# Kernel optimization log

Measured on AMD Instinct MI355X. Metric: run time of the kernel, lower is better.

The kernel has to match this reference:

```python
import math
import jax, jax.numpy as jnp
import numpy as np

B, S, D, H = 2, 2048, 2048, 16  # batch, seq, d_model, n_heads


def setup_inputs() -> dict:
    key = jax.random.key(0)
    ks = jax.random.split(key, 5)
    w_scale = 1.0 / math.sqrt(D)
    return {
        "x": jax.random.normal(ks[0], (B, S, D), jnp.float32),
        "attn_bias": jax.random.normal(ks[1], (1, H, S, S), jnp.float32) * 0.1,
        "Wqkv_w": jax.random.normal(ks[2], (3 * D, D), jnp.float32) * w_scale,
        "Wqkv_b": jnp.zeros((3 * D,), jnp.float32),
        "out_w": jax.random.normal(ks[3], (D, D), jnp.float32) * w_scale,
        "out_b": jnp.zeros((D,), jnp.float32),
    }


def reference(x, attn_bias, Wqkv_w, Wqkv_b, out_w, out_b):
    b, s, d = x.shape
    hd = d // H                      # head dim = 128
    scale = 1.0 / math.sqrt(hd)      # module default: 1/sqrt(d_model // n_heads)

    # fused QKV projection
    qkv = x @ Wqkv_w.T + Wqkv_b                       # [b, s, 3d]
    q, k, v = jnp.split(qkv, 3, axis=2)               # each [b, s, d]
    q = q.reshape(b, s, H, hd).transpose(0, 2, 1, 3)  # [b, h, s, hd]
    k = k.reshape(b, s, H, hd).transpose(0, 2, 1, 3)
    v = v.reshape(b, s, H, hd).transpose(0, 2, 1, 3)

    # scaled scores + additive bias (bias sliced to trailing q/k lengths)
    scores = jnp.einsum('bhqd,bhkd->bhqk', q, k) * scale
    scores = scores + attn_bias[:, :, -s:, -s:]

    # causal mask, masked positions set to dtype min (matches masked_fill with finfo.min)
    causal = jnp.tril(jnp.ones((s, s), dtype=bool))   # True = keep
    min_val = jnp.finfo(scores.dtype).min
    scores = jnp.where(causal[None, None, :, :], scores, min_val)

    p = jax.nn.softmax(scores, axis=-1)               # [b, h, s, s]
    out = jnp.einsum('bhqk,bhkd->bhqd', p, v)         # [b, h, s, hd]
    out = out.transpose(0, 2, 1, 3).reshape(b, s, d)  # [b, s, d]

    return out @ out_w.T + out_b
```

## Files before the change

### kernel.cpp

```cpp
#include <hip/hip_runtime.h>
#include <hip/hip_bf16.h>
#include <stdint.h>

#define H_  16
#define S_  2048
#define D_  2048
#define HD_ 128

typedef __bf16 bf16x8 __attribute__((ext_vector_type(8)));
typedef short  s16x8  __attribute__((ext_vector_type(8)));
typedef float  f32x4  __attribute__((ext_vector_type(4)));
typedef unsigned short u16x4 __attribute__((ext_vector_type(4)));

__device__ __forceinline__ unsigned short f2bf(float f) {
    unsigned u = __builtin_bit_cast(unsigned, f);
    u += 0x7fffu + ((u >> 16) & 1u);
    return (unsigned short)(u >> 16);
}

__device__ __forceinline__ bf16x8 ld_bf8(const unsigned short* p) {
    s16x8 r = *reinterpret_cast<const s16x8*>(p);
    return __builtin_bit_cast(bf16x8, r);
}

#define GLOAD_LDS16(gp, lp)                                                     \
    __builtin_amdgcn_global_load_lds(                                            \
        (const __attribute__((address_space(1))) void*)(gp),                     \
        (__attribute__((address_space(3))) void*)(lp), 16, 0, 0)

__global__ __launch_bounds__(256) void cast_f32_bf16(const float* __restrict__ in,
                                                     unsigned short* __restrict__ out,
                                                     int n) {
    int i = (blockIdx.x * 256 + threadIdx.x) * 4;
    if (i >= n) return;
    float4 v = *reinterpret_cast<const float4*>(in + i);
    u16x4 o;
    o[0] = f2bf(v.x); o[1] = f2bf(v.y); o[2] = f2bf(v.z); o[3] = f2bf(v.w);
    *reinterpret_cast<u16x4*>(out + i) = o;
}

__global__ __launch_bounds__(256) void gemm_bt_qkv(const unsigned short* __restrict__ A,
                                                   const unsigned short* __restrict__ W,
                                                   const float* __restrict__ bias,
                                                   unsigned short* __restrict__ Qo,
                                                   unsigned short* __restrict__ Ko,
                                                   unsigned short* __restrict__ Vo) {
    __shared__ alignas(16) unsigned short As[128 * 32];
    __shared__ alignas(16) unsigned short Bs[128 * 32];
    const int t  = threadIdx.x;
    const int l  = t & 63, w = t >> 6;
    const int wr = w >> 1, wc = w & 1;
    const int lr = l & 15, g = l >> 4;

    const int GX = 48, NWG = 1536, CPX = NWG / 8;
    const int raw = blockIdx.y * GX + blockIdx.x;
    const int swz = (raw & 7) * CPX + (raw >> 3);
    const int m0 = (swz / GX) * 128, n0 = (swz % GX) * 128;
    const int Kd = D_;

    f32x4 zero = {0.f, 0.f, 0.f, 0.f};
    f32x4 acc[4][4];
    for (int i = 0; i < 4; ++i)
        for (int j = 0; j < 4; ++j) acc[i][j] = zero;

    const int ea = t * 8;
    const int rowA = ea >> 5, colA = ea & 31;

    for (int kt = 0; kt < Kd; kt += 32) {
        GLOAD_LDS16(A + (size_t)(m0 + rowA) * Kd + kt + colA, &As[ea]);
        GLOAD_LDS16(A + (size_t)(m0 + 64 + rowA) * Kd + kt + colA, &As[2048 + ea]);
        GLOAD_LDS16(W + (size_t)(n0 + rowA) * Kd + kt + colA, &Bs[ea]);
        GLOAD_LDS16(W + (size_t)(n0 + 64 + rowA) * Kd + kt + colA, &Bs[2048 + ea]);
        __syncthreads();
        bf16x8 af[4], bfr[4];
        for (int mi = 0; mi < 4; ++mi) af[mi]  = ld_bf8(&As[(wr * 64 + mi * 16 + lr) * 32 + g * 8]);
        for (int ni = 0; ni < 4; ++ni) bfr[ni] = ld_bf8(&Bs[(wc * 64 + ni * 16 + lr) * 32 + g * 8]);
        for (int mi = 0; mi < 4; ++mi)
            for (int ni = 0; ni < 4; ++ni)
                acc[mi][ni] = __builtin_amdgcn_mfma_f32_16x16x32_bf16(af[mi], bfr[ni], acc[mi][ni], 0, 0, 0);
        __syncthreads();
    }

    for (int mi = 0; mi < 4; ++mi) {
        for (int ni = 0; ni < 4; ++ni) {
            for (int i = 0; i < 4; ++i) {
                int m = m0 + wr * 64 + mi * 16 + g * 4 + i;
                int n = n0 + wc * 64 + ni * 16 + lr;
                float v = acc[mi][ni][i] + bias[n];
                int which = n >> 11;
                int n2 = n & 2047;
                int h = n2 >> 7, d = n2 & 127;
                int b = m >> 11, s = m & 2047;
                unsigned short bv = f2bf(v);
                if (which == 0)
                    Qo[(((size_t)(b * H_ + h)) * S_ + s) * HD_ + d] = bv;
                else if (which == 1)
                    Ko[(((size_t)(b * H_ + h)) * S_ + s) * HD_ + d] = bv;
                else
                    Vo[(((size_t)(b * H_ + h)) * HD_ + d) * S_ + s] = bv;
            }
        }
    }
}

__global__ __launch_bounds__(256) void attn_kernel10(const unsigned short* __restrict__ Q,
                                                     const unsigned short* __restrict__ K,
                                                     const unsigned short* __restrict__ Vt,
                                                     const float* __restrict__ biasPtr,
                                                     unsigned short* __restrict__ O) {
    __shared__ alignas(16) unsigned short Klds[2][4096];
    __shared__ alignas(16) unsigned short Vlds[2][4096];
    __shared__ alignas(16) unsigned short Pbuf[4][16 * 32];

    const int t  = threadIdx.x;
    const int l  = t & 63, w = t >> 6;
    const int lr = l & 15, g = l >> 4;

    const int raw   = blockIdx.x;
    const int xcd   = raw & 7;
    const int local = raw >> 3;
    const int cu    = local & 31;
    const int slot  = local >> 5;
    const int qt    = (slot & 1) ? cu : (31 - cu);
    const int bh    = xcd + 8 * slot;
    const int b     = bh >> 4, head = bh & 15;

    const unsigned short* Qb = Q + (size_t)bh * S_ * HD_;
    const unsigned short* Kb = K + (size_t)bh * S_ * HD_;
    const unsigned short* Vb = Vt + (size_t)bh * HD_ * S_;
    const float* Bh32 = biasPtr + (size_t)head * S_ * S_;
    const float scale = 0.08838834764831845f;

    const int q0 = qt * 64 + w * 16;

    bf16x8 qf[4];
#pragma unroll
    for (int dc = 0; dc < 4; ++dc)
        qf[dc] = ld_bf8(Qb + (size_t)(q0 + lr) * HD_ + dc * 32 + g * 8);

    f32x4 zero = {0.f, 0.f, 0.f, 0.f};
    f32x4 o[8];
#pragma unroll
    for (int nc = 0; nc < 8; ++nc) o[nc] = zero;
    float lp[4] = {0.f, 0.f, 0.f, 0.f};

    unsigned short* Pw = Pbuf[w];

    auto STAGE = [&](int buf, int k0) {
#pragma unroll
        for (int p = 0; p < 2; ++p) {
            int lin = p * 4096 + t * 16;
            int row = lin >> 8;
            int colb = lin & 255;
            int scolb = colb ^ ((row & 7) << 4);
            GLOAD_LDS16(Kb + (size_t)(k0 + row) * HD_ + (scolb >> 1), &Klds[buf][lin >> 1]);
        }
#pragma unroll
        for (int p = 0; p < 2; ++p) {
            int lin = p * 4096 + t * 16;
            int row = lin >> 6;
            int colb = lin & 63;
            int scolb = colb ^ ((row & 3) << 4);
            GLOAD_LDS16(Vb + (size_t)row * S_ + k0 + (scolb >> 1), &Vlds[buf][lin >> 1]);
        }
    };

    STAGE(0, 0);
    __syncthreads();

    const int nch = 2 * qt + 2;
    int cur = 0;
    for (int c = 0; c < nch; ++c) {
        const int k0 = c * 32;

        if (c + 1 < nch) STAGE(cur ^ 1, k0 + 32);

        float bias_r[4][2];
#pragma unroll
        for (int i = 0; i < 4; ++i) {
            const int boff = (q0 + g * 4 + i) * S_ + k0 + lr;
#pragma unroll
            for (int kc = 0; kc < 2; ++kc)
                bias_r[i][kc] = Bh32[boff + kc * 16];
        }

        f32x4 s[2];
        s[0] = zero; s[1] = zero;
#pragma unroll
        for (int kc = 0; kc < 2; ++kc) {
            bf16x8 kf[4];
#pragma unroll
            for (int dc = 0; dc < 4; ++dc)
                kf[dc] = ld_bf8(&Klds[cur][(kc * 16 + lr) * 128 + ((dc * 32 + g * 8) ^ ((lr & 7) << 3))]);
#pragma unroll
            for (int dc = 0; dc < 4; ++dc)
                s[kc] = __builtin_amdgcn_mfma_f32_16x16x32_bf16(qf[dc], kf[dc], s[kc], 0, 0, 0);
        }

        const bool maskzone = (c >= nch - 2);
#pragma unroll
        for (int i = 0; i < 4; ++i) {
            const int rowabs = q0 + g * 4 + i;
            const int prow   = g * 4 + i;
            float e[2];
#pragma unroll
            for (int kc = 0; kc < 2; ++kc) {
                float v = s[kc][i] * scale + bias_r[i][kc];
                if (maskzone && (k0 + kc * 16 + lr > rowabs)) v = -1.0e30f;
                e[kc] = __expf(v - 16.0f);
            }
            lp[i] += e[0] + e[1];
            const int sw = (prow & 3) << 3;
            Pw[(prow * 32 + 0  + lr) ^ sw] = f2bf(e[0]);
            Pw[(prow * 32 + 16 + lr) ^ sw] = f2bf(e[1]);
        }

        {
            bf16x8 pa = ld_bf8(&Pw[lr * 32 + ((g * 8) ^ ((lr & 3) << 3))]);
#pragma unroll
            for (int nc = 0; nc < 8; ++nc) {
                bf16x8 vf = ld_bf8(&Vlds[cur][(nc * 16 + lr) * 32 + ((g * 8) ^ ((lr & 3) << 3))]);
                o[nc] = __builtin_amdgcn_mfma_f32_16x16x32_bf16(pa, vf, o[nc], 0, 0, 0);
            }
        }

        __syncthreads();
        cur ^= 1;
    }

#pragma unroll
    for (int i = 0; i < 4; ++i) {
        lp[i] += __shfl_xor(lp[i], 1);
        lp[i] += __shfl_xor(lp[i], 2);
        lp[i] += __shfl_xor(lp[i], 4);
        lp[i] += __shfl_xor(lp[i], 8);
    }

#pragma unroll
    for (int i = 0; i < 4; ++i) {
        float inv = 1.0f / lp[i];
        int row = q0 + g * 4 + i;
#pragma unroll
        for (int nc = 0; nc < 8; ++nc) {
            O[((size_t)(b * S_ + row)) * D_ + head * HD_ + nc * 16 + lr] = f2bf(o[nc][i] * inv);
        }
    }
}

__global__ __launch_bounds__(256) void gemm_bt_out(const unsigned short* __restrict__ A,
                                                   const unsigned short* __restrict__ W,
                                                   const float* __restrict__ bias,
                                                   float* __restrict__ out) {
    __shared__ alignas(16) unsigned short As[128 * 32];
    __shared__ alignas(16) unsigned short Bs[128 * 32];
    const int t  = threadIdx.x;
    const int l  = t & 63, w = t >> 6;
    const int wr = w >> 1, wc = w & 1;
    const int lr = l & 15, g = l >> 4;

    const int GX = 16, NWG = 512, CPX = NWG / 8;
    const int raw = blockIdx.y * GX + blockIdx.x;
    const int swz = (raw & 7) * CPX + (raw >> 3);
    const int m0 = (swz / GX) * 128, n0 = (swz % GX) * 128;
    const int Kd = D_;

    f32x4 zero = {0.f, 0.f, 0.f, 0.f};
    f32x4 acc[4][4];
    for (int i = 0; i < 4; ++i)
        for (int j = 0; j < 4; ++j) acc[i][j] = zero;

    const int ea = t * 8;
    const int rowA = ea >> 5, colA = ea & 31;

    for (int kt = 0; kt < Kd; kt += 32) {
        GLOAD_LDS16(A + (size_t)(m0 + rowA) * Kd + kt + colA, &As[ea]);
        GLOAD_LDS16(A + (size_t)(m0 + 64 + rowA) * Kd + kt + colA, &As[2048 + ea]);
        GLOAD_LDS16(W + (size_t)(n0 + rowA) * Kd + kt + colA, &Bs[ea]);
        GLOAD_LDS16(W + (size_t)(n0 + 64 + rowA) * Kd + kt + colA, &Bs[2048 + ea]);
        __syncthreads();
        bf16x8 af[4], bfr[4];
        for (int mi = 0; mi < 4; ++mi) af[mi]  = ld_bf8(&As[(wr * 64 + mi * 16 + lr) * 32 + g * 8]);
        for (int ni = 0; ni < 4; ++ni) bfr[ni] = ld_bf8(&Bs[(wc * 64 + ni * 16 + lr) * 32 + g * 8]);
        for (int mi = 0; mi < 4; ++mi)
            for (int ni = 0; ni < 4; ++ni)
                acc[mi][ni] = __builtin_amdgcn_mfma_f32_16x16x32_bf16(af[mi], bfr[ni], acc[mi][ni], 0, 0, 0);
        __syncthreads();
    }

    for (int mi = 0; mi < 4; ++mi) {
        for (int ni = 0; ni < 4; ++ni) {
            for (int i = 0; i < 4; ++i) {
                int m = m0 + wr * 64 + mi * 16 + g * 4 + i;
                int n = n0 + wc * 64 + ni * 16 + lr;
                out[(size_t)m * D_ + n] = acc[mi][ni][i] + bias[n];
            }
        }
    }
}

extern "C" void kernel_launch(void* const* d_in, const int* in_sizes, int n_in,
                              void* d_out, int out_size, void* d_ws, size_t ws_size,
                              hipStream_t stream) {
    (void)in_sizes; (void)n_in; (void)out_size; (void)ws_size;
    const float* x         = (const float*)d_in[0];
    const float* attn_bias = (const float*)d_in[1];
    const float* Wqkv_w    = (const float*)d_in[2];
    const float* Wqkv_b    = (const float*)d_in[3];
    const float* out_w     = (const float*)d_in[4];
    const float* out_b     = (const float*)d_in[5];
    float* out = (float*)d_out;

    char* ws = (char*)d_ws;
    unsigned short* xb    = (unsigned short*)(ws);
    unsigned short* wqkvb = (unsigned short*)(ws + 16777216);
    unsigned short* woutb = (unsigned short*)(ws + 41943040);
    unsigned short* Qb    = (unsigned short*)(ws + 50331648);
    unsigned short* Kb    = (unsigned short*)(ws + 67108864);
    unsigned short* Vtb   = (unsigned short*)(ws + 83886080);
    unsigned short* Ob    = xb;

    cast_f32_bf16<<<8192, 256, 0, stream>>>(x, xb, 8388608);
    cast_f32_bf16<<<12288, 256, 0, stream>>>(Wqkv_w, wqkvb, 12582912);
    cast_f32_bf16<<<4096, 256, 0, stream>>>(out_w, woutb, 4194304);
    gemm_bt_qkv<<<dim3(48, 32), 256, 0, stream>>>(xb, wqkvb, Wqkv_b, Qb, Kb, Vtb);
    attn_kernel10<<<1024, 256, 0, stream>>>(Qb, Kb, Vtb, attn_bias, Ob);
    gemm_bt_out<<<dim3(16, 32), 256, 0, stream>>>(Ob, woutb, out_b, out);
}
```

Before: 325.2 us.

## Rewrite GEMMs with triple-buffered async LDS pipeline, swizzled layout, larger tiles

Both projection GEMMs now share a core that loads 64-wide K slices into three rotating LDS buffers through global_load_lds. It waits with partial vmcnt, so global loads for two tiles ahead overlap the MFMA work and only one barrier is needed per iteration. The LDS rows are XOR-swizzled to avoid bank conflicts on fragment reads, and the block tile grows to 256x128 with 512 threads. In exchange, LDS use rises to about 144 KB per block, which limits occupancy to one block per CU and leaves fewer blocks for the out-projection to fill the GPU.

```diff
diff --git a/kernel.cpp b/kernel.cpp
--- a/kernel.cpp
+++ b/kernel.cpp
@@ -39,58 +39,112 @@
     *reinterpret_cast<u16x4*>(out + i) = o;
 }
 
-__global__ __launch_bounds__(256) void gemm_bt_qkv(const unsigned short* __restrict__ A,
-                                                   const unsigned short* __restrict__ W,
-                                                   const float* __restrict__ bias,
-                                                   unsigned short* __restrict__ Qo,
-                                                   unsigned short* __restrict__ Ko,
-                                                   unsigned short* __restrict__ Vo) {
-    __shared__ alignas(16) unsigned short As[128 * 32];
-    __shared__ alignas(16) unsigned short Bs[128 * 32];
+__device__ __forceinline__ void gemm3_core(const unsigned short* __restrict__ Aptr,
+                                           const unsigned short* __restrict__ Bptr,
+                                           int m0, int n0, f32x4 acc[4][4]) {
+    __shared__ alignas(16) unsigned short As3[3][256 * 64];
+    __shared__ alignas(16) unsigned short Bs3[3][128 * 64];
     const int t  = threadIdx.x;
     const int l  = t & 63, w = t >> 6;
-    const int wr = w >> 1, wc = w & 1;
+    const int wm = w >> 1, wn = w & 1;
     const int lr = l & 15, g = l >> 4;
 
-    const int GX = 48, NWG = 1536, CPX = NWG / 8;
-    const int raw = blockIdx.y * GX + blockIdx.x;
-    const int swz = (raw & 7) * CPX + (raw >> 3);
-    const int m0 = (swz / GX) * 128, n0 = (swz % GX) * 128;
-    const int Kd = D_;
-
     f32x4 zero = {0.f, 0.f, 0.f, 0.f};
+#pragma unroll
+    for (int i = 0; i < 4; ++i)
+#pragma unroll
+        for (int j = 0; j < 4; ++j) acc[i][j] = zero;
+
+    auto STAGE = [&](int buf, int kt) {
+#pragma unroll
+        for (int p = 0; p < 4; ++p) {
+            int lin = (p * 512 + t) * 16;
+            int row = lin >> 7, colb = lin & 127;
+            int scol = (colb ^ ((row & 7) << 4)) >> 1;
+            GLOAD_LDS16(Aptr + (size_t)(m0 + row) * D_ + kt + scol, &As3[buf][lin >> 1]);
+        }
+#pragma unroll
+        for (int p = 0; p < 2; ++p) {
+            int lin = (p * 512 + t) * 16;
+            int row = lin >> 7, colb = lin & 127;
+            int scol = (colb ^ ((row & 7) << 4)) >> 1;
+            GLOAD_LDS16(Bptr + (size_t)(n0 + row) * D_ + kt + scol, &Bs3[buf][lin >> 1]);
+        }
+    };
+
+    STAGE(0, 0);
+    STAGE(1, 64);
+    asm volatile("s_waitcnt vmcnt(6)" ::: "memory");
+    __builtin_amdgcn_s_barrier();
+
+    const int NT = D_ / 64;
+    int bsel = 0;
+    for (int tt = 0; tt < NT; ++tt) {
+        int s2 = bsel + 2; if (s2 >= 3) s2 -= 3;
+        if (tt + 2 < NT) STAGE(s2, (tt + 2) * 64);
+
+        const unsigned short* Ab = As3[bsel];
+        const unsigned short* Bb = Bs3[bsel];
+        bf16x8 af[4][2], bfr[4][2];
+#pragma unroll
+        for (int mi = 0; mi < 4; ++mi)
+#pragma unroll
+            for (int ks = 0; ks < 2; ++ks)
+                af[mi][ks] = ld_bf8(&Ab[(wm * 64 + mi * 16 + lr) * 64 +
+                                        ((ks * 32 + g * 8) ^ ((lr & 7) << 3))]);
+#pragma unroll
+        for (int ni = 0; ni < 4; ++ni)
+#pragma unroll
+            for (int ks = 0; ks < 2; ++ks)
+                bfr[ni][ks] = ld_bf8(&Bb[(wn * 64 + ni * 16 + lr) * 64 +
+                                         ((ks * 32 + g * 8) ^ ((lr & 7) << 3))]);
+#pragma unroll
+        for (int ks = 0; ks < 2; ++ks)
+#pragma unroll
+            for (int mi = 0; mi < 4; ++mi)
+#pragma unroll
+                for (int ni = 0; ni < 4; ++ni)
+                    acc[mi][ni] = __builtin_amdgcn_mfma_f32_16x16x32_bf16(
+                        af[mi][ks], bfr[ni][ks], acc[mi][ni], 0, 0, 0);
+
+        if (tt + 1 < NT) {
+            if (tt + 2 < NT) { asm volatile("s_waitcnt vmcnt(6)" ::: "memory"); }
+            else             { asm volatile("s_waitcnt vmcnt(0)" ::: "memory"); }
+            __builtin_amdgcn_s_barrier();
+        }
+        ++bsel; if (bsel == 3) bsel = 0;
+    }
+}
+
+__global__ __launch_bounds__(512) void gemm3_qkv(const unsigned short* __restrict__ Aptr,
+                                                 const unsigned short* __restrict__ Bptr,
+                                                 const float* __restrict__ bias,
+                                                 unsigned short* __restrict__ Qo,
+                                                 unsigned short* __restrict__ Ko,
+                                                 unsigned short* __restrict__ Vo) {
+    const int raw = blockIdx.x;
+    const int swz = (raw & 7) * 96 + (raw >> 3);
+    const int m0 = (swz / 48) * 256, n0 = (swz % 48) * 128;
+
     f32x4 acc[4][4];
-    for (int i = 0; i < 4; ++i)
-        for (int j = 0; j < 4; ++j) acc[i][j] = zero;
-
-    const int ea = t * 8;
-    const int rowA = ea >> 5, colA = ea & 31;
-
-    for (int kt = 0; kt < Kd; kt += 32) {
-        GLOAD_LDS16(A + (size_t)(m0 + rowA) * Kd + kt + colA, &As[ea]);
-        GLOAD_LDS16(A + (size_t)(m0 + 64 + rowA) * Kd + kt + colA, &As[2048 + ea]);
-        GLOAD_LDS16(W + (size_t)(n0 + rowA) * Kd + kt + colA, &Bs[ea]);
-        GLOAD_LDS16(W + (size_t)(n0 + 64 + rowA) * Kd + kt + colA, &Bs[2048 + ea]);
-        __syncthreads();
-        bf16x8 af[4], bfr[4];
-        for (int mi = 0; mi < 4; ++mi) af[mi]  = ld_bf8(&As[(wr * 64 + mi * 16 + lr) * 32 + g * 8]);
-        for (int ni = 0; ni < 4; ++ni) bfr[ni] = ld_bf8(&Bs[(wc * 64 + ni * 16 + lr) * 32 + g * 8]);
-        for (int mi = 0; mi < 4; ++mi)
-            for (int ni = 0; ni < 4; ++ni)
-                acc[mi][ni] = __builtin_amdgcn_mfma_f32_16x16x32_bf16(af[mi], bfr[ni], acc[mi][ni], 0, 0, 0);
-        __syncthreads();
-    }
+    gemm3_core(Aptr, Bptr, m0, n0, acc);
+
+    const int l  = threadIdx.x & 63, w = threadIdx.x >> 6;
+    const int wm = w >> 1, wn = w & 1;
+    const int lr = l & 15, g = l >> 4;
 
     for (int mi = 0; mi < 4; ++mi) {
         for (int ni = 0; ni < 4; ++ni) {
             for (int i = 0; i < 4; ++i) {
-                int m = m0 + wr * 64 + mi * 16 + g * 4 + i;
-                int n = n0 + wc * 64 + ni * 16 + lr;
+                int m = m0 + wm * 64 + mi * 16 + g * 4 + i;
+                int n = n0 + wn * 64 + ni * 16 + lr;
                 float v = acc[mi][ni][i] + bias[n];
                 int which = n >> 11;
                 int n2 = n & 2047;
-                int h = n2 >> 7, d = n2 & 127;
-                int b = m >> 11, s = m & 2047;
+                int h = n2 >> 7;
+                int d = n2 & 127;
+                int b = m >> 11;
+                int s = m & 2047;
                 unsigned short bv = f2bf(v);
                 if (which == 0)
                     Qo[(((size_t)(b * H_ + h)) * S_ + s) * HD_ + d] = bv;
@@ -98,6 +152,32 @@
                     Ko[(((size_t)(b * H_ + h)) * S_ + s) * HD_ + d] = bv;
                 else
                     Vo[(((size_t)(b * H_ + h)) * HD_ + d) * S_ + s] = bv;
+            }
+        }
+    }
+}
+
+__global__ __launch_bounds__(512) void gemm3_out(const unsigned short* __restrict__ Aptr,
+                                                 const unsigned short* __restrict__ Bptr,
+                                                 const float* __restrict__ bias,
+                                                 float* __restrict__ out) {
+    const int raw = blockIdx.x;
+    const int swz = (raw & 7) * 32 + (raw >> 3);
+    const int m0 = (swz / 16) * 256, n0 = (swz % 16) * 128;
+
+    f32x4 acc[4][4];
+    gemm3_core(Aptr, Bptr, m0, n0, acc);
+
+    const int l  = threadIdx.x & 63, w = threadIdx.x >> 6;
+    const int wm = w >> 1, wn = w & 1;
+    const int lr = l & 15, g = l >> 4;
+
+    for (int mi = 0; mi < 4; ++mi) {
+        for (int ni = 0; ni < 4; ++ni) {
+            for (int i = 0; i < 4; ++i) {
+                int m = m0 + wm * 64 + mi * 16 + g * 4 + i;
+                int n = n0 + wn * 64 + ni * 16 + lr;
+                out[(size_t)m * D_ + n] = acc[mi][ni][i] + bias[n];
             }
         }
     }
@@ -243,57 +323,6 @@
 #pragma unroll
         for (int nc = 0; nc < 8; ++nc) {
             O[((size_t)(b * S_ + row)) * D_ + head * HD_ + nc * 16 + lr] = f2bf(o[nc][i] * inv);
-        }
-    }
-}
-
-__global__ __launch_bounds__(256) void gemm_bt_out(const unsigned short* __restrict__ A,
-                                                   const unsigned short* __restrict__ W,
-                                                   const float* __restrict__ bias,
-                                                   float* __restrict__ out) {
-    __shared__ alignas(16) unsigned short As[128 * 32];
-    __shared__ alignas(16) unsigned short Bs[128 * 32];
-    const int t  = threadIdx.x;
-    const int l  = t & 63, w = t >> 6;
-    const int wr = w >> 1, wc = w & 1;
-    const int lr = l & 15, g = l >> 4;
-
-    const int GX = 16, NWG = 512, CPX = NWG / 8;
-    const int raw = blockIdx.y * GX + blockIdx.x;
-    const int swz = (raw & 7) * CPX + (raw >> 3);
-    const int m0 = (swz / GX) * 128, n0 = (swz % GX) * 128;
-    const int Kd = D_;
-
-    f32x4 zero = {0.f, 0.f, 0.f, 0.f};
-    f32x4 acc[4][4];
-    for (int i = 0; i < 4; ++i)
-        for (int j = 0; j < 4; ++j) acc[i][j] = zero;
-
-    const int ea = t * 8;
-    const int rowA = ea >> 5, colA = ea & 31;
-
-    for (int kt = 0; kt < Kd; kt += 32) {
-        GLOAD_LDS16(A + (size_t)(m0 + rowA) * Kd + kt + colA, &As[ea]);
-        GLOAD_LDS16(A + (size_t)(m0 + 64 + rowA) * Kd + kt + colA, &As[2048 + ea]);
-        GLOAD_LDS16(W + (size_t)(n0 + rowA) * Kd + kt + colA, &Bs[ea]);
-        GLOAD_LDS16(W + (size_t)(n0 + 64 + rowA) * Kd + kt + colA, &Bs[2048 + ea]);
-        __syncthreads();
-        bf16x8 af[4], bfr[4];
-        for (int mi = 0; mi < 4; ++mi) af[mi]  = ld_bf8(&As[(wr * 64 + mi * 16 + lr) * 32 + g * 8]);
-        for (int ni = 0; ni < 4; ++ni) bfr[ni] = ld_bf8(&Bs[(wc * 64 + ni * 16 + lr) * 32 + g * 8]);
-        for (int mi = 0; mi < 4; ++mi)
-            for (int ni = 0; ni < 4; ++ni)
-                acc[mi][ni] = __builtin_amdgcn_mfma_f32_16x16x32_bf16(af[mi], bfr[ni], acc[mi][ni], 0, 0, 0);
-        __syncthreads();
-    }
-
-    for (int mi = 0; mi < 4; ++mi) {
-        for (int ni = 0; ni < 4; ++ni) {
-            for (int i = 0; i < 4; ++i) {
-                int m = m0 + wr * 64 + mi * 16 + g * 4 + i;
-                int n = n0 + wc * 64 + ni * 16 + lr;
-                out[(size_t)m * D_ + n] = acc[mi][ni][i] + bias[n];
-            }
         }
     }
 }
@@ -322,7 +351,7 @@
     cast_f32_bf16<<<8192, 256, 0, stream>>>(x, xb, 8388608);
     cast_f32_bf16<<<12288, 256, 0, stream>>>(Wqkv_w, wqkvb, 12582912);
     cast_f32_bf16<<<4096, 256, 0, stream>>>(out_w, woutb, 4194304);
-    gemm_bt_qkv<<<dim3(48, 32), 256, 0, stream>>>(xb, wqkvb, Wqkv_b, Qb, Kb, Vtb);
+    gemm3_qkv<<<768, 512, 0, stream>>>(xb, wqkvb, Wqkv_b, Qb, Kb, Vtb);
     attn_kernel10<<<1024, 256, 0, stream>>>(Qb, Kb, Vtb, attn_bias, Ob);
-    gemm_bt_out<<<dim3(16, 32), 256, 0, stream>>>(Ob, woutb, out_b, out);
-}
+    gemm3_out<<<256, 512, 0, stream>>>(Ob, woutb, out_b, out);
+}
```

After: 354.6 us. +9.0%, slower.

## Share GEMM core with BK=64 XOR-swizzled LDS and vectorize V-transpose stores

Applied to the files above, without the earlier changes.

Both projection GEMMs now use a shared core that stages 64-wide K tiles instead of 32, halving the number of barrier pairs per tile. The LDS layout uses an XOR swizzle on 16-byte chunks to reduce bank conflicts on fragment reads. The QKV epilogue hoists the head/batch decode and bias loads, and writes transposed V as 4-element vector stores. LDS use per block doubles, which may lower occupancy.

```diff
diff --git a/kernel.cpp b/kernel.cpp
--- a/kernel.cpp
+++ b/kernel.cpp
@@ -39,65 +39,147 @@
     *reinterpret_cast<u16x4*>(out + i) = o;
 }
 
+__device__ __forceinline__ void gemm128_core(const unsigned short* __restrict__ Aptr,
+                                             const unsigned short* __restrict__ Bptr,
+                                             int m0, int n0,
+                                             unsigned short* As, unsigned short* Bs,
+                                             f32x4 acc[4][4]) {
+    const int t  = threadIdx.x;
+    const int l  = t & 63, w = t >> 6;
+    const int wr = w >> 1, wc = w & 1;
+    const int lr = l & 15, g = l >> 4;
+
+    f32x4 zero = {0.f, 0.f, 0.f, 0.f};
+#pragma unroll
+    for (int i = 0; i < 4; ++i)
+#pragma unroll
+        for (int j = 0; j < 4; ++j) acc[i][j] = zero;
+
+    for (int kt = 0; kt < D_; kt += 64) {
+#pragma unroll
+        for (int p = 0; p < 4; ++p) {
+            int lin = (p * 256 + t) * 16;
+            int row = lin >> 7, colb = lin & 127;
+            int scol = (colb ^ ((row & 7) << 4)) >> 1;
+            GLOAD_LDS16(Aptr + (size_t)(m0 + row) * D_ + kt + scol, &As[lin >> 1]);
+        }
+#pragma unroll
+        for (int p = 0; p < 4; ++p) {
+            int lin = (p * 256 + t) * 16;
+            int row = lin >> 7, colb = lin & 127;
+            int scol = (colb ^ ((row & 7) << 4)) >> 1;
+            GLOAD_LDS16(Bptr + (size_t)(n0 + row) * D_ + kt + scol, &Bs[lin >> 1]);
+        }
+        __syncthreads();
+#pragma unroll
+        for (int ks = 0; ks < 2; ++ks) {
+            bf16x8 af[4], bfr[4];
+#pragma unroll
+            for (int mi = 0; mi < 4; ++mi)
+                af[mi] = ld_bf8(&As[(wr * 64 + mi * 16 + lr) * 64 +
+                                    ((ks * 32 + g * 8) ^ ((lr & 7) << 3))]);
+#pragma unroll
+            for (int ni = 0; ni < 4; ++ni)
+                bfr[ni] = ld_bf8(&Bs[(wc * 64 + ni * 16 + lr) * 64 +
+                                     ((ks * 32 + g * 8) ^ ((lr & 7) << 3))]);
+#pragma unroll
+            for (int mi = 0; mi < 4; ++mi)
+#pragma unroll
+                for (int ni = 0; ni < 4; ++ni)
+                    acc[mi][ni] = __builtin_amdgcn_mfma_f32_16x16x32_bf16(
+                        af[mi], bfr[ni], acc[mi][ni], 0, 0, 0);
+        }
+        __syncthreads();
+    }
+}
+
 __global__ __launch_bounds__(256) void gemm_bt_qkv(const unsigned short* __restrict__ A,
                                                    const unsigned short* __restrict__ W,
                                                    const float* __restrict__ bias,
                                                    unsigned short* __restrict__ Qo,
                                                    unsigned short* __restrict__ Ko,
                                                    unsigned short* __restrict__ Vo) {
-    __shared__ alignas(16) unsigned short As[128 * 32];
-    __shared__ alignas(16) unsigned short Bs[128 * 32];
-    const int t  = threadIdx.x;
-    const int l  = t & 63, w = t >> 6;
-    const int wr = w >> 1, wc = w & 1;
-    const int lr = l & 15, g = l >> 4;
+    __shared__ alignas(16) unsigned short As[128 * 64];
+    __shared__ alignas(16) unsigned short Bs[128 * 64];
 
     const int GX = 48, NWG = 1536, CPX = NWG / 8;
     const int raw = blockIdx.y * GX + blockIdx.x;
     const int swz = (raw & 7) * CPX + (raw >> 3);
     const int m0 = (swz / GX) * 128, n0 = (swz % GX) * 128;
-    const int Kd = D_;
-
-    f32x4 zero = {0.f, 0.f, 0.f, 0.f};
+
     f32x4 acc[4][4];
-    for (int i = 0; i < 4; ++i)
-        for (int j = 0; j < 4; ++j) acc[i][j] = zero;
-
-    const int ea = t * 8;
-    const int rowA = ea >> 5, colA = ea & 31;
-
-    for (int kt = 0; kt < Kd; kt += 32) {
-        GLOAD_LDS16(A + (size_t)(m0 + rowA) * Kd + kt + colA, &As[ea]);
-        GLOAD_LDS16(A + (size_t)(m0 + 64 + rowA) * Kd + kt + colA, &As[2048 + ea]);
-        GLOAD_LDS16(W + (size_t)(n0 + rowA) * Kd + kt + colA, &Bs[ea]);
-        GLOAD_LDS16(W + (size_t)(n0 + 64 + rowA) * Kd + kt + colA, &Bs[2048 + ea]);
-        __syncthreads();
-        bf16x8 af[4], bfr[4];
-        for (int mi = 0; mi < 4; ++mi) af[mi]  = ld_bf8(&As[(wr * 64 + mi * 16 + lr) * 32 + g * 8]);
-        for (int ni = 0; ni < 4; ++ni) bfr[ni] = ld_bf8(&Bs[(wc * 64 + ni * 16 + lr) * 32 + g * 8]);
-        for (int mi = 0; mi < 4; ++mi)
-            for (int ni = 0; ni < 4; ++ni)
-                acc[mi][ni] = __builtin_amdgcn_mfma_f32_16x16x32_bf16(af[mi], bfr[ni], acc[mi][ni], 0, 0, 0);
-        __syncthreads();
-    }
+    gemm128_core(A, W, m0, n0, As, Bs, acc);
+
+    const int l  = threadIdx.x & 63, w = threadIdx.x >> 6;
+    const int wr = w >> 1, wc = w & 1;
+    const int lr = l & 15, g = l >> 4;
+
+    const int which = n0 >> 11;
+    const int h     = (n0 & 2047) >> 7;
+    const int b     = m0 >> 11;
+    const int sb    = m0 & 2047;
+
+    float bias_v[4];
+#pragma unroll
+    for (int ni = 0; ni < 4; ++ni)
+        bias_v[ni] = bias[n0 + wc * 64 + ni * 16 + lr];
+
+    if (which == 2) {
+        unsigned short* Vb = Vo + ((size_t)(b * H_ + h)) * HD_ * S_;
+#pragma unroll
+        for (int mi = 0; mi < 4; ++mi) {
+#pragma unroll
+            for (int ni = 0; ni < 4; ++ni) {
+                int d = wc * 64 + ni * 16 + lr;
+                int s = sb + wr * 64 + mi * 16 + g * 4;
+                u16x4 pv;
+#pragma unroll
+                for (int i = 0; i < 4; ++i) pv[i] = f2bf(acc[mi][ni][i] + bias_v[ni]);
+                *reinterpret_cast<u16x4*>(&Vb[(size_t)d * S_ + s]) = pv;
+            }
+        }
+    } else {
+        unsigned short* Pb = ((which == 0) ? Qo : Ko) + ((size_t)(b * H_ + h)) * S_ * HD_;
+#pragma unroll
+        for (int mi = 0; mi < 4; ++mi) {
+#pragma unroll
+            for (int ni = 0; ni < 4; ++ni) {
+                int d = wc * 64 + ni * 16 + lr;
+#pragma unroll
+                for (int i = 0; i < 4; ++i) {
+                    int s = sb + wr * 64 + mi * 16 + g * 4 + i;
+                    Pb[(size_t)s * HD_ + d] = f2bf(acc[mi][ni][i] + bias_v[ni]);
+                }
+            }
+        }
+    }
+}
+
+__global__ __launch_bounds__(256) void gemm_bt_out(const unsigned short* __restrict__ A,
+                                                   const unsigned short* __restrict__ W,
+                                                   const float* __restrict__ bias,
+                                                   float* __restrict__ out) {
+    __shared__ alignas(16) unsigned short As[128 * 64];
+    __shared__ alignas(16) unsigned short Bs[128 * 64];
+
+    const int GX = 16, NWG = 512, CPX = NWG / 8;
+    const int raw = blockIdx.y * GX + blockIdx.x;
+    const int swz = (raw & 7) * CPX + (raw >> 3);
+    const int m0 = (swz / GX) * 128, n0 = (swz % GX) * 128;
+
+    f32x4 acc[4][4];
+    gemm128_core(A, W, m0, n0, As, Bs, acc);
+
+    const int l  = threadIdx.x & 63, w = threadIdx.x >> 6;
+    const int wr = w >> 1, wc = w & 1;
+    const int lr = l & 15, g = l >> 4;
 
     for (int mi = 0; mi < 4; ++mi) {
         for (int ni = 0; ni < 4; ++ni) {
             for (int i = 0; i < 4; ++i) {
                 int m = m0 + wr * 64 + mi * 16 + g * 4 + i;
                 int n = n0 + wc * 64 + ni * 16 + lr;
-                float v = acc[mi][ni][i] + bias[n];
-                int which = n >> 11;
-                int n2 = n & 2047;
-                int h = n2 >> 7, d = n2 & 127;
-                int b = m >> 11, s = m & 2047;
-                unsigned short bv = f2bf(v);
-                if (which == 0)
-                    Qo[(((size_t)(b * H_ + h)) * S_ + s) * HD_ + d] = bv;
-                else if (which == 1)
-                    Ko[(((size_t)(b * H_ + h)) * S_ + s) * HD_ + d] = bv;
-                else
-                    Vo[(((size_t)(b * H_ + h)) * HD_ + d) * S_ + s] = bv;
+                out[(size_t)m * D_ + n] = acc[mi][ni][i] + bias[n];
             }
         }
     }
@@ -243,57 +325,6 @@
 #pragma unroll
         for (int nc = 0; nc < 8; ++nc) {
             O[((size_t)(b * S_ + row)) * D_ + head * HD_ + nc * 16 + lr] = f2bf(o[nc][i] * inv);
-        }
-    }
-}
-
-__global__ __launch_bounds__(256) void gemm_bt_out(const unsigned short* __restrict__ A,
-                                                   const unsigned short* __restrict__ W,
-                                                   const float* __restrict__ bias,
-                                                   float* __restrict__ out) {
-    __shared__ alignas(16) unsigned short As[128 * 32];
-    __shared__ alignas(16) unsigned short Bs[128 * 32];
-    const int t  = threadIdx.x;
-    const int l  = t & 63, w = t >> 6;
-    const int wr = w >> 1, wc = w & 1;
-    const int lr = l & 15, g = l >> 4;
-
-    const int GX = 16, NWG = 512, CPX = NWG / 8;
-    const int raw = blockIdx.y * GX + blockIdx.x;
-    const int swz = (raw & 7) * CPX + (raw >> 3);
-    const int m0 = (swz / GX) * 128, n0 = (swz % GX) * 128;
-    const int Kd = D_;
-
-    f32x4 zero = {0.f, 0.f, 0.f, 0.f};
-    f32x4 acc[4][4];
-    for (int i = 0; i < 4; ++i)
-        for (int j = 0; j < 4; ++j) acc[i][j] = zero;
-
-    const int ea = t * 8;
-    const int rowA = ea >> 5, colA = ea & 31;
-
-    for (int kt = 0; kt < Kd; kt += 32) {
-        GLOAD_LDS16(A + (size_t)(m0 + rowA) * Kd + kt + colA, &As[ea]);
-        GLOAD_LDS16(A + (size_t)(m0 + 64 + rowA) * Kd + kt + colA, &As[2048 + ea]);
-        GLOAD_LDS16(W + (size_t)(n0 + rowA) * Kd + kt + colA, &Bs[ea]);
-        GLOAD_LDS16(W + (size_t)(n0 + 64 + rowA) * Kd + kt + colA, &Bs[2048 + ea]);
-        __syncthreads();
-        bf16x8 af[4], bfr[4];
-        for (int mi = 0; mi < 4; ++mi) af[mi]  = ld_bf8(&As[(wr * 64 + mi * 16 + lr) * 32 + g * 8]);
-        for (int ni = 0; ni < 4; ++ni) bfr[ni] = ld_bf8(&Bs[(wc * 64 + ni * 16 + lr) * 32 + g * 8]);
-        for (int mi = 0; mi < 4; ++mi)
-            for (int ni = 0; ni < 4; ++ni)
-                acc[mi][ni] = __builtin_amdgcn_mfma_f32_16x16x32_bf16(af[mi], bfr[ni], acc[mi][ni], 0, 0, 0);
-        __syncthreads();
-    }
-
-    for (int mi = 0; mi < 4; ++mi) {
-        for (int ni = 0; ni < 4; ++ni) {
-            for (int i = 0; i < 4; ++i) {
-                int m = m0 + wr * 64 + mi * 16 + g * 4 + i;
-                int n = n0 + wc * 64 + ni * 16 + lr;
-                out[(size_t)m * D_ + n] = acc[mi][ni][i] + bias[n];
-            }
         }
     }
 }
```

Measured after the change: 310.1 us, median of 2. 1.05x faster.
